# Kernel optimization log

Hardware: AMD Instinct MI355X
Metric: run time of the kernel (lower is better)

The kernel has to match this reference:

```python
import jax, jax.numpy as jnp
import numpy as np

HEADS = 8
DIM_HEAD = 32
EPS = 1e-5


def _rel_index(h, w):
    # matches Attention._generate_relative_index (static, computed on host)
    coords = np.stack(np.meshgrid(np.arange(h), np.arange(w), indexing='ij')).reshape(2, -1)
    rel = coords[:, :, None] - coords[:, None, :]  # [2, n, n]
    rel[0] += h - 1
    rel[1] += w - 1
    rel[0] *= 2 * w - 1
    idx = rel.sum(0).reshape(-1)
    # torch.clamp(relative_index, 0, max_index) -- indices are already in range here
    return jnp.asarray(np.clip(idx, 0, (2 * h - 1) * (2 * w - 1) - 1))


def _layernorm(x, g, b):
    m = jnp.mean(x, axis=-1, keepdims=True)
    v = jnp.var(x, axis=-1, keepdims=True)
    return (x - m) * jax.lax.rsqrt(v + EPS) * g + b


def setup_inputs() -> dict:
    key = jax.random.key(0)
    ks = jax.random.split(key, 6)
    B, C, H, W = 64, 384, 16, 16
    inner = HEADS * DIM_HEAD  # 256
    hid = 4 * C               # 1536
    def nrm(k, shape, s=0.02):
        return jax.random.normal(k, shape, jnp.float32) * s
    return {
        'x': jax.random.normal(ks[0], (B, C, H, W), jnp.float32),
        'ln1_g': jnp.ones((C,), jnp.float32),
        'ln1_b': jnp.zeros((C,), jnp.float32),
        'w_qkv': nrm(ks[1], (C, 3 * inner)),
        'bias_table': nrm(ks[2], ((2 * H - 1) * (2 * W - 1), HEADS)),
        'w_out': nrm(ks[3], (inner, C)),
        'b_out': jnp.zeros((C,), jnp.float32),
        'ln2_g': jnp.ones((C,), jnp.float32),
        'ln2_b': jnp.zeros((C,), jnp.float32),
        'w_ff1': nrm(ks[4], (C, hid)),
        'b_ff1': jnp.zeros((hid,), jnp.float32),
        'w_ff2': nrm(ks[5], (hid, C)),
        'b_ff2': jnp.zeros((C,), jnp.float32),
    }


def reference(x, ln1_g, ln1_b, w_qkv, bias_table, w_out, b_out,
              ln2_g, ln2_b, w_ff1, b_ff1, w_ff2, b_ff2):
    B, C, H, W = x.shape
    n = H * W
    t = x.reshape(B, C, n).transpose(0, 2, 1)  # [B, n, C]

    # --- attention branch (PreNorm(LayerNorm) -> Attention) ---
    a = _layernorm(t, ln1_g, ln1_b)
    qkv = a @ w_qkv  # [B, n, 3*inner]
    q, k, v = jnp.split(qkv, 3, axis=-1)
    def split_heads(z):
        return z.reshape(B, n, HEADS, DIM_HEAD).transpose(0, 2, 1, 3)  # [B, h, n, d]
    q, k, v = split_heads(q), split_heads(k), split_heads(v)
    dots = jnp.einsum('bhid,bhjd->bhij', q, k) * (DIM_HEAD ** -0.5)
    idx = _rel_index(H, W)  # [n*n]
    rel_bias = bias_table[idx].reshape(n, n, HEADS).transpose(2, 0, 1)[None]  # [1, h, n, n]
    attn = jax.nn.softmax(dots + rel_bias, axis=-1)
    o = jnp.einsum('bhij,bhjd->bhid', attn, v)
    o = o.transpose(0, 2, 1, 3).reshape(B, n, HEADS * DIM_HEAD)
    attn_out = o @ w_out + b_out  # to_out Linear (dropout=0)

    # --- feedforward branch (PreNorm(LayerNorm) -> FFN) ---
    f = _layernorm(t, ln2_g, ln2_b)
    f = jax.nn.gelu(f @ w_ff1 + b_ff1, approximate=False) @ w_ff2 + b_ff2

    y = t + attn_out + f  # x_adjusted + attn_out + ff_out
    return y.transpose(0, 2, 1).reshape(B, C, H, W)
```

## Files before the change

kernel.cpp:

```cpp
#include <hip/hip_runtime.h>

typedef __bf16 bf16;
typedef __bf16 bf16x8 __attribute__((ext_vector_type(8)));
typedef float f32x4 __attribute__((ext_vector_type(4)));

__device__ __forceinline__ void gll16(const void* g, void* l) {
    __builtin_amdgcn_global_load_lds((const __attribute__((address_space(1))) void*)g,
                                     (__attribute__((address_space(3))) void*)l, 16, 0, 0);
}

__device__ __forceinline__ float gelu_f(float v) {
    float x2 = v * v;
    float sn = v * fmaf(-0.0713540072f, x2, -1.5957691216f);
    float e  = __expf(sn);
    return v * __builtin_amdgcn_rcpf(1.0f + e);
}

__launch_bounds__(256)
__global__ void prep_kernel(const float* __restrict__ wqkv, const float* __restrict__ wout,
                            const float* __restrict__ wff1, const float* __restrict__ wff2,
                            bf16* __restrict__ wqkvT, bf16* __restrict__ woutT,
                            bf16* __restrict__ wff1T, bf16* __restrict__ wff2T,
                            const float* __restrict__ x,
                            const float* __restrict__ g1, const float* __restrict__ b1,
                            const float* __restrict__ g2, const float* __restrict__ b2,
                            bf16* __restrict__ a, bf16* __restrict__ f) {
    __shared__ __align__(16) float smem[12672 + 512 + 64];
    const int tid = threadIdx.x;
    int g = blockIdx.x;
    if (g < 1536) {
        float (*tl)[33] = (float (*)[33])smem;
        const float* in; bf16* out; int R, Cc, bx, by;
        if (g < 288)       { in = wqkv; out = wqkvT; R = 384;  Cc = 768;  bx = g % 24; by = g / 24; }
        else if (g < 384)  { g -= 288; in = wout; out = woutT; R = 256;  Cc = 384;  bx = g % 12; by = g / 12; }
        else if (g < 960)  { g -= 384; in = wff1; out = wff1T; R = 384;  Cc = 1536; bx = g % 48; by = g / 48; }
        else               { g -= 960; in = wff2; out = wff2T; R = 1536; Cc = 384;  bx = g % 12; by = g / 12; }
        const int c0 = bx * 32, r0 = by * 32;
        const int cl = tid & 31, r8 = tid >> 5;
#pragma unroll
        for (int k = 0; k < 4; k++) {
            int r = k * 8 + r8;
            tl[r][cl] = in[(size_t)(r0 + r) * Cc + c0 + cl];
        }
        __syncthreads();
#pragma unroll
        for (int k = 0; k < 4; k++) {
            int cc = k * 8 + r8;
            out[(size_t)(c0 + cc) * R + r0 + cl] = (bf16)tl[cl][cc];
        }
        return;
    }
    g -= 1536;
    float (*tile)[33] = (float (*)[33])smem;
    float (*S)[32]  = (float (*)[32])(smem + 12672);
    float (*SS)[32] = (float (*)[32])(smem + 12928);
    float* Mn = smem + 13184;
    float* Rs = smem + 13216;
    const int bb = g >> 3;
    const int i0 = (g & 7) * 32;
    {
        const int i_l = tid & 31, c_l = tid >> 5;
        const size_t base = (size_t)bb * 384 * 256 + i0 + i_l;
#pragma unroll 6
        for (int c = c_l; c < 384; c += 8)
            tile[c][i_l] = x[base + (size_t)c * 256];
    }
    __syncthreads();
    {
        const int i_s = tid & 31, p = tid >> 5;
        float s = 0.f, ss = 0.f;
#pragma unroll 6
        for (int j = 0; j < 48; j++) {
            float v = tile[p * 48 + j][i_s];
            s += v; ss += v * v;
        }
        S[p][i_s] = s; SS[p][i_s] = ss;
    }
    __syncthreads();
    if (tid < 32) {
        float t1 = 0.f, t2 = 0.f;
#pragma unroll
        for (int p = 0; p < 8; p++) { t1 += S[p][tid]; t2 += SS[p][tid]; }
        float mean = t1 * (1.0f / 384.0f);
        float var  = t2 * (1.0f / 384.0f) - mean * mean;
        Mn[tid] = mean;
        Rs[tid] = rsqrtf(var + 1e-5f);
    }
    __syncthreads();
    const int lane = tid & 63, w = tid >> 6;
#pragma unroll
    for (int rr = 0; rr < 8; rr++) {
        const int i = w * 8 + rr;
        const float mean = Mn[i], rstd = Rs[i];
        const size_t orow = ((size_t)bb * 256 + i0 + i) * 384;
#pragma unroll
        for (int pass = 0; pass < 6; pass++) {
            const int c = pass * 64 + lane;
            float nh = (tile[c][i] - mean) * rstd;
            a[orow + c] = (bf16)(nh * g1[c] + b1[c]);
            f[orow + c] = (bf16)(nh * g2[c] + b2[c]);
        }
    }
}

template <int EPI>
__launch_bounds__(256)
__global__ void gemm_bt(const bf16* __restrict__ A, const bf16* __restrict__ Bt,
                        const float* __restrict__ bias, bf16* __restrict__ C,
                        int M, int N, int K, int nx) {
    __shared__ bf16 lds[16384];
    bf16* lA = lds;
    bf16* lB = lds + 4096;
    const int tid = threadIdx.x;
    const int g = blockIdx.x;
    const int x = (g >> 3) % nx;
    const int y = (g & 7) + 8 * (g / (8 * nx));
    const int m0 = y * 128, n0 = x * 128;
    const int lane = tid & 63, w = tid >> 6;
    const int l16 = lane & 15, quad = lane >> 4;
    const int wm = (w & 1) * 64, wn = (w >> 1) * 64;

    f32x4 zero = {0.f, 0.f, 0.f, 0.f};
    f32x4 acc[4][4];
#pragma unroll
    for (int i = 0; i < 4; i++)
#pragma unroll
        for (int j = 0; j < 4; j++) acc[i][j] = zero;

    const int c0 = tid, c1 = tid + 256;
    const int r0 = c0 >> 2, k0c = (c0 & 3) * 8;
    const int r1 = c1 >> 2, k1c = (c1 & 3) * 8;
    const bf16* Abase = A + (size_t)m0 * K;
    const bf16* Bbase = Bt + (size_t)n0 * K;

    for (int kb = 0; kb < K; kb += 32) {
        gll16(Abase + (size_t)r0 * K + kb + k0c, lA + c0 * 8);
        gll16(Abase + (size_t)r1 * K + kb + k1c, lA + c1 * 8);
        gll16(Bbase + (size_t)r0 * K + kb + k0c, lB + c0 * 8);
        gll16(Bbase + (size_t)r1 * K + kb + k1c, lB + c1 * 8);
        __syncthreads();
        bf16x8 af[4], bfr[4];
#pragma unroll
        for (int i = 0; i < 4; i++)
            af[i] = *(const bf16x8*)(lA + (wm + i * 16 + l16) * 32 + quad * 8);
#pragma unroll
        for (int j = 0; j < 4; j++)
            bfr[j] = *(const bf16x8*)(lB + (wn + j * 16 + l16) * 32 + quad * 8);
#pragma unroll
        for (int i = 0; i < 4; i++)
#pragma unroll
            for (int j = 0; j < 4; j++)
                acc[i][j] = __builtin_amdgcn_mfma_f32_16x16x32_bf16(af[i], bfr[j], acc[i][j], 0, 0, 0);
        __syncthreads();
    }

#pragma unroll
    for (int j = 0; j < 4; j++) {
        const int col = wn + j * 16 + l16;
        float bv = 0.f;
        if (EPI >= 1) bv = bias[n0 + col];
#pragma unroll
        for (int i = 0; i < 4; i++) {
            const int row0 = wm + i * 16 + quad * 4;
#pragma unroll
            for (int r = 0; r < 4; r++) {
                float v = acc[i][j][r] + bv;
                if (EPI == 2) v = gelu_f(v);
                lds[(row0 + r) * 128 + col] = (bf16)v;
            }
        }
    }
    __syncthreads();
#pragma unroll
    for (int it = 0; it < 8; it++) {
        const int ch = tid + it * 256;
        const int row = ch >> 4, cc = (ch & 15) * 8;
        *(bf16x8*)(C + (size_t)(m0 + row) * N + n0 + cc) = *(const bf16x8*)(lds + row * 128 + cc);
    }
}

#define GEMM64_PROLOGUE_AND_KLOOP                                                   \
    const int tid = threadIdx.x;                                                    \
    const int g = blockIdx.x;                                                       \
    const int x_ = (g >> 3) % nx;                                                   \
    const int y_ = (g & 7) + 8 * (g / (8 * nx));                                    \
    const int m0 = y_ * 128, n0 = x_ * 64;                                          \
    const int lane = tid & 63, w = tid >> 6;                                        \
    const int l16 = lane & 15, quad = lane >> 4;                                    \
    const int wm = (w & 1) * 64, wn = (w >> 1) * 32;                                \
    f32x4 zero = {0.f, 0.f, 0.f, 0.f};                                              \
    f32x4 acc[4][2];                                                                \
    _Pragma("unroll") for (int i = 0; i < 4; i++)                                   \
        _Pragma("unroll") for (int j = 0; j < 2; j++) acc[i][j] = zero;             \
    const int c0 = tid, c1 = tid + 256;                                             \
    const int r0 = c0 >> 2, k0c = (c0 & 3) * 8;                                     \
    const int r1 = c1 >> 2, k1c = (c1 & 3) * 8;                                     \
    const bf16* Abase = A + (size_t)m0 * K;                                         \
    const bf16* Bbase = Bt + (size_t)n0 * K;                                        \
    for (int kb = 0; kb < K; kb += 64) {                                            \
        gll16(Abase + (size_t)r0 * K + kb + k0c,      lA0 + c0 * 8);                \
        gll16(Abase + (size_t)r1 * K + kb + k1c,      lA0 + c1 * 8);                \
        gll16(Abase + (size_t)r0 * K + kb + 32 + k0c, lA1 + c0 * 8);                \
        gll16(Abase + (size_t)r1 * K + kb + 32 + k1c, lA1 + c1 * 8);                \
        gll16(Bbase + (size_t)r0 * K + kb + k0c,      lB0 + c0 * 8);                \
        gll16(Bbase + (size_t)r0 * K + kb + 32 + k0c, lB1 + c0 * 8);                \
        __syncthreads();                                                            \
        bf16x8 af[4], bfr[2];                                                       \
        _Pragma("unroll") for (int i = 0; i < 4; i++)                               \
            af[i] = *(const bf16x8*)(lA0 + (wm + i * 16 + l16) * 32 + quad * 8);    \
        _Pragma("unroll") for (int j = 0; j < 2; j++)                               \
            bfr[j] = *(const bf16x8*)(lB0 + (wn + j * 16 + l16) * 32 + quad * 8);   \
        _Pragma("unroll") for (int i = 0; i < 4; i++)                               \
            _Pragma("unroll") for (int j = 0; j < 2; j++)                           \
                acc[i][j] = __builtin_amdgcn_mfma_f32_16x16x32_bf16(af[i], bfr[j], acc[i][j], 0, 0, 0); \
        _Pragma("unroll") for (int i = 0; i < 4; i++)                               \
            af[i] = *(const bf16x8*)(lA1 + (wm + i * 16 + l16) * 32 + quad * 8);    \
        _Pragma("unroll") for (int j = 0; j < 2; j++)                               \
            bfr[j] = *(const bf16x8*)(lB1 + (wn + j * 16 + l16) * 32 + quad * 8);   \
        _Pragma("unroll") for (int i = 0; i < 4; i++)                               \
            _Pragma("unroll") for (int j = 0; j < 2; j++)                           \
                acc[i][j] = __builtin_amdgcn_mfma_f32_16x16x32_bf16(af[i], bfr[j], acc[i][j], 0, 0, 0); \
        __syncthreads();                                                            \
    }

__launch_bounds__(256)
__global__ void gemm_bt_tr64(const bf16* __restrict__ A, const bf16* __restrict__ Bt,
                             const float* __restrict__ bias, bf16* __restrict__ Ct,
                             int M, int N, int K, int nx) {
    __shared__ bf16 lds[12288];
    bf16* lA0 = lds;
    bf16* lA1 = lds + 4096;
    bf16* lB0 = lds + 8192;
    bf16* lB1 = lds + 10240;
    GEMM64_PROLOGUE_AND_KLOOP
#pragma unroll
    for (int j = 0; j < 2; j++) {
        const int col = wn + j * 16 + l16;
        const float bv = bias[n0 + col];
#pragma unroll
        for (int i = 0; i < 4; i++) {
            const int row0 = wm + i * 16 + quad * 4;
#pragma unroll
            for (int r = 0; r < 4; r++)
                lds[col * 132 + row0 + r] = (bf16)(acc[i][j][r] + bv);
        }
    }
    __syncthreads();
    const int b = m0 >> 8, ib = m0 & 255;
#pragma unroll
    for (int it = 0; it < 4; it++) {
        const int ch = tid + it * 256;
        const int cl = ch >> 4, ic = (ch & 15) * 8;
        *(bf16x8*)(Ct + ((size_t)(b * 384 + n0 + cl) * 256 + ib + ic)) =
            *(const bf16x8*)(lds + cl * 132 + ic);
    }
}

__launch_bounds__(256)
__global__ void gemm_bt_final64(const bf16* __restrict__ A, const bf16* __restrict__ Bt,
                                const float* __restrict__ bias,
                                const float* __restrict__ xres, const bf16* __restrict__ attn_t,
                                float* __restrict__ out, int M, int N, int K, int nx) {
    __shared__ bf16 lds[12288];
    bf16* lA0 = lds;
    bf16* lA1 = lds + 4096;
    bf16* lB0 = lds + 8192;
    bf16* lB1 = lds + 10240;
    GEMM64_PROLOGUE_AND_KLOOP
#pragma unroll
    for (int j = 0; j < 2; j++) {
        const int col = wn + j * 16 + l16;
        const float bv = bias[n0 + col];
#pragma unroll
        for (int i = 0; i < 4; i++) {
            const int row0 = wm + i * 16 + quad * 4;
#pragma unroll
            for (int r = 0; r < 4; r++)
                lds[col * 132 + row0 + r] = (bf16)(acc[i][j][r] + bv);
        }
    }
    __syncthreads();
    const int b = m0 >> 8, ib = m0 & 255;
#pragma unroll
    for (int it = 0; it < 4; it++) {
        const int ch = tid + it * 256;
        const int cl = ch >> 4, ic = (ch & 15) * 8;
        const size_t base = (size_t)(b * 384 + n0 + cl) * 256 + ib + ic;
        bf16x8 ff = *(const bf16x8*)(lds + cl * 132 + ic);
        bf16x8 at = *(const bf16x8*)(attn_t + base);
#pragma unroll
        for (int e = 0; e < 8; e++)
            out[base + e] = xres[base + e] + (float)at[e] + (float)ff[e];
    }
}

__launch_bounds__(256)
__global__ void attn_kernel(const bf16* __restrict__ qkv,
                            const float* __restrict__ btab,
                            bf16* __restrict__ o) {
    __shared__ float sbias[961];
    __shared__ __align__(16) bf16 sK[256 * 32];
    __shared__ __align__(16) bf16 sVt[32][264];
    __shared__ __align__(16) bf16 sP[4][16][264];
    const int tid = threadIdx.x;
    const int g = blockIdx.x;
    const int h  = (g >> 3) & 7;
    const int bb = (g & 7) + 8 * (g >> 6);
    const int lane = tid & 63, w = tid >> 6;
    const int l16 = lane & 15, quad = lane >> 4;
    const size_t qkvb = (size_t)bb * 256 * 768;
    const bf16* Qbase = qkv + qkvb + h * 32;
    const bf16* Kbase = qkv + qkvb + 256 + h * 32;
    const bf16* Vbase = qkv + qkvb + 512 + h * 32;

    for (int e = tid; e < 961; e += 256) sbias[e] = btab[e * 8 + h];
#pragma unroll
    for (int it = 0; it < 4; it++) {
        const int ch = it * 256 + tid;
        const int row = ch >> 2, d8 = (ch & 3) * 8;
        gll16(Kbase + (size_t)row * 768 + d8, sK + ch * 8);
    }
#pragma unroll
    for (int it = 0; it < 4; it++) {
        const int ch = it * 256 + tid;
        const int k = ch >> 2, d8 = (ch & 3) * 8;
        bf16x8 vv = *(const bf16x8*)(Vbase + (size_t)k * 768 + d8);
#pragma unroll
        for (int j = 0; j < 8; j++)
            sVt[d8 + j][k] = vv[j];
    }
    __syncthreads();

    f32x4 zero = {0.f, 0.f, 0.f, 0.f};
    for (int qc = 0; qc < 4; qc++) {
        const int qbase = qc * 64 + w * 16;
        bf16x8 qf = *(const bf16x8*)(Qbase + (size_t)(qbase + l16) * 768 + quad * 8);
        f32x4 s[16];
#pragma unroll
        for (int kt = 0; kt < 16; kt++) {
            bf16x8 kf = *(const bf16x8*)(sK + (kt * 16 + l16) * 32 + quad * 8);
            s[kt] = __builtin_amdgcn_mfma_f32_16x16x32_bf16(qf, kf, zero, 0, 0, 0);
        }
        const int qi0 = qbase + quad * 4;
        float mx[4] = {-1e30f, -1e30f, -1e30f, -1e30f};
#pragma unroll
        for (int kt = 0; kt < 16; kt++) {
            const int j = kt * 16 + l16;
            const int yj = j >> 4, xj = j & 15;
#pragma unroll
            for (int r = 0; r < 4; r++) {
                const int q = qi0 + r;
                const int tix = ((q >> 4) - yj + 15) * 31 + ((q & 15) - xj + 15);
                float v = s[kt][r] * 0.17677669529663687f + sbias[tix];
                s[kt][r] = v;
                mx[r] = fmaxf(mx[r], v);
            }
        }
#pragma unroll
        for (int r = 0; r < 4; r++)
            for (int msk = 1; msk < 16; msk <<= 1)
                mx[r] = fmaxf(mx[r], __shfl_xor(mx[r], msk, 64));
        float sum[4] = {0.f, 0.f, 0.f, 0.f};
#pragma unroll
        for (int kt = 0; kt < 16; kt++)
#pragma unroll
            for (int r = 0; r < 4; r++) {
                float e = __expf(s[kt][r] - mx[r]);
                s[kt][r] = e;
                sum[r] += e;
            }
#pragma unroll
        for (int r = 0; r < 4; r++) {
            for (int msk = 1; msk < 16; msk <<= 1)
                sum[r] += __shfl_xor(sum[r], msk, 64);
            sum[r] = 1.0f / sum[r];
        }
#pragma unroll
        for (int kt = 0; kt < 16; kt++)
#pragma unroll
            for (int r = 0; r < 4; r++)
                sP[w][quad * 4 + r][kt * 16 + l16] = (bf16)(s[kt][r] * sum[r]);
        f32x4 oacc[2];
        oacc[0] = zero; oacc[1] = zero;
#pragma unroll
        for (int ks = 0; ks < 8; ks++) {
            bf16x8 pf = *(const bf16x8*)(&sP[w][l16][ks * 32 + quad * 8]);
#pragma unroll
            for (int dt = 0; dt < 2; dt++) {
                bf16x8 vf = *(const bf16x8*)(&sVt[dt * 16 + l16][ks * 32 + quad * 8]);
                oacc[dt] = __builtin_amdgcn_mfma_f32_16x16x32_bf16(pf, vf, oacc[dt], 0, 0, 0);
            }
        }
#pragma unroll
        for (int dt = 0; dt < 2; dt++)
#pragma unroll
            for (int r = 0; r < 4; r++)
                o[(size_t)(bb * 256 + qbase + quad * 4 + r) * 256 + h * 32 + dt * 16 + l16] = (bf16)oacc[dt][r];
    }
}

extern "C" void kernel_launch(void* const* d_in, const int* in_sizes, int n_in,
                              void* d_out, int out_size, void* d_ws, size_t ws_size,
                              hipStream_t stream) {
    const float* x    = (const float*)d_in[0];
    const float* g1   = (const float*)d_in[1];
    const float* b1   = (const float*)d_in[2];
    const float* wqkv = (const float*)d_in[3];
    const float* btab = (const float*)d_in[4];
    const float* wout = (const float*)d_in[5];
    const float* bout = (const float*)d_in[6];
    const float* g2   = (const float*)d_in[7];
    const float* b2   = (const float*)d_in[8];
    const float* wff1 = (const float*)d_in[9];
    const float* bff1 = (const float*)d_in[10];
    const float* wff2 = (const float*)d_in[11];
    const float* bff2 = (const float*)d_in[12];
    float* out = (float*)d_out;

    bf16* ws = (bf16*)d_ws;
    const size_t NA = 6291456;
    bf16* wqkvT = ws;
    bf16* woutT = wqkvT + 294912;
    bf16* wff1T = woutT + 98304;
    bf16* wff2T = wff1T + 589824;
    bf16* f_buf    = ws + 1572864;
    bf16* attn_t   = f_buf + NA;
    bf16* R        = attn_t + NA;
    bf16* a_buf    = R;
    bf16* qkv_buf  = R + NA;
    bf16* o_buf    = R;
    bf16* ffh_buf  = R;

    dim3 b256(256);
    prep_kernel<<<2048, b256, 0, stream>>>(wqkv, wout, wff1, wff2, wqkvT, woutT, wff1T, wff2T,
                                           x, g1, b1, g2, b2, a_buf, f_buf);

    gemm_bt<0><<<6 * 128, b256, 0, stream>>>(a_buf, wqkvT, nullptr, qkv_buf, 16384, 768, 384, 6);
    attn_kernel<<<512, b256, 0, stream>>>(qkv_buf, btab, o_buf);
    gemm_bt_tr64<<<6 * 128, b256, 0, stream>>>(o_buf, woutT, bout, attn_t, 16384, 384, 256, 6);
    gemm_bt<2><<<12 * 128, b256, 0, stream>>>(f_buf, wff1T, bff1, ffh_buf, 16384, 1536, 384, 12);
    gemm_bt_final64<<<6 * 128, b256, 0, stream>>>(ffh_buf, wff2T, bff2, x, attn_t, out,
                                                  16384, 384, 1536, 6);
}
```

Baseline: 228.8 us.

## Double-buffer LDS staging in GEMM kernels and vectorize final residual store

Converts the GEMM k-loops to double-buffered LDS staging. The next 32-wide K slice is issued via global_load_lds before the MFMA work on the current slice, which removes one barrier per iteration and overlaps load latency with compute. The 64-wide GEMMs drop their 64-deep K step for 32-deep steps with ping-pong buffers. The final epilogue also switches to float4 loads and stores for the residual sum. The risk is that async LDS loads may not be properly awaited before use: the compiler's vmcnt waits and the single barrier must cover the in-flight buffer.

```diff
diff --git a/kernel.cpp b/kernel.cpp
--- a/kernel.cpp
+++ b/kernel.cpp
@@ -109,8 +109,6 @@
                         const float* __restrict__ bias, bf16* __restrict__ C,
                         int M, int N, int K, int nx) {
     __shared__ bf16 lds[16384];
-    bf16* lA = lds;
-    bf16* lB = lds + 4096;
     const int tid = threadIdx.x;
     const int g = blockIdx.x;
     const int x = (g >> 3) % nx;
@@ -133,12 +131,23 @@
     const bf16* Abase = A + (size_t)m0 * K;
     const bf16* Bbase = Bt + (size_t)n0 * K;
 
+#define STAGE128(buf, kb)                                                   \
+    {                                                                       \
+        bf16* lA = lds + (buf) * 8192;                                      \
+        bf16* lB = lA + 4096;                                               \
+        gll16(Abase + (size_t)r0 * K + (kb) + k0c, lA + c0 * 8);            \
+        gll16(Abase + (size_t)r1 * K + (kb) + k1c, lA + c1 * 8);            \
+        gll16(Bbase + (size_t)r0 * K + (kb) + k0c, lB + c0 * 8);            \
+        gll16(Bbase + (size_t)r1 * K + (kb) + k1c, lB + c1 * 8);            \
+    }
+
+    STAGE128(0, 0);
+    __syncthreads();
+    int cur = 0;
     for (int kb = 0; kb < K; kb += 32) {
-        gll16(Abase + (size_t)r0 * K + kb + k0c, lA + c0 * 8);
-        gll16(Abase + (size_t)r1 * K + kb + k1c, lA + c1 * 8);
-        gll16(Bbase + (size_t)r0 * K + kb + k0c, lB + c0 * 8);
-        gll16(Bbase + (size_t)r1 * K + kb + k1c, lB + c1 * 8);
-        __syncthreads();
+        if (kb + 32 < K) STAGE128(cur ^ 1, kb + 32);
+        const bf16* lA = lds + cur * 8192;
+        const bf16* lB = lA + 4096;
         bf16x8 af[4], bfr[4];
 #pragma unroll
         for (int i = 0; i < 4; i++)
@@ -152,7 +161,9 @@
             for (int j = 0; j < 4; j++)
                 acc[i][j] = __builtin_amdgcn_mfma_f32_16x16x32_bf16(af[i], bfr[j], acc[i][j], 0, 0, 0);
         __syncthreads();
-    }
+        cur ^= 1;
+    }
+#undef STAGE128
 
 #pragma unroll
     for (int j = 0; j < 4; j++) {
@@ -195,32 +206,35 @@
     const int c0 = tid, c1 = tid + 256;                                             \
     const int r0 = c0 >> 2, k0c = (c0 & 3) * 8;                                     \
     const int r1 = c1 >> 2, k1c = (c1 & 3) * 8;                                     \
+    const int rB = tid >> 2, kBc = (tid & 3) * 8;                                   \
     const bf16* Abase = A + (size_t)m0 * K;                                         \
     const bf16* Bbase = Bt + (size_t)n0 * K;                                        \
-    for (int kb = 0; kb < K; kb += 64) {                                            \
-        gll16(Abase + (size_t)r0 * K + kb + k0c,      lA0 + c0 * 8);                \
-        gll16(Abase + (size_t)r1 * K + kb + k1c,      lA0 + c1 * 8);                \
-        gll16(Abase + (size_t)r0 * K + kb + 32 + k0c, lA1 + c0 * 8);                \
-        gll16(Abase + (size_t)r1 * K + kb + 32 + k1c, lA1 + c1 * 8);                \
-        gll16(Bbase + (size_t)r0 * K + kb + k0c,      lB0 + c0 * 8);                \
-        gll16(Bbase + (size_t)r0 * K + kb + 32 + k0c, lB1 + c0 * 8);                \
-        __syncthreads();                                                            \
+    STAGE64(0, 0);                                                                  \
+    __syncthreads();                                                                \
+    int cur = 0;                                                                    \
+    for (int kb = 0; kb < K; kb += 32) {                                            \
+        if (kb + 32 < K) STAGE64(cur ^ 1, kb + 32);                                 \
+        const bf16* lA = lds + cur * 6144;                                          \
+        const bf16* lB = lA + 4096;                                                 \
         bf16x8 af[4], bfr[2];                                                       \
         _Pragma("unroll") for (int i = 0; i < 4; i++)                               \
-            af[i] = *(const bf16x8*)(lA0 + (wm + i * 16 + l16) * 32 + quad * 8);    \
+            af[i] = *(const bf16x8*)(lA + (wm + i * 16 + l16) * 32 + quad * 8);     \
         _Pragma("unroll") for (int j = 0; j < 2; j++)                               \
-            bfr[j] = *(const bf16x8*)(lB0 + (wn + j * 16 + l16) * 32 + quad * 8);   \
-        _Pragma("unroll") for (int i = 0; i < 4; i++)                               \
-            _Pragma("unroll") for (int j = 0; j < 2; j++)                           \
-                acc[i][j] = __builtin_amdgcn_mfma_f32_16x16x32_bf16(af[i], bfr[j], acc[i][j], 0, 0, 0); \
-        _Pragma("unroll") for (int i = 0; i < 4; i++)                               \
-            af[i] = *(const bf16x8*)(lA1 + (wm + i * 16 + l16) * 32 + quad * 8);    \
-        _Pragma("unroll") for (int j = 0; j < 2; j++)                               \
-            bfr[j] = *(const bf16x8*)(lB1 + (wn + j * 16 + l16) * 32 + quad * 8);   \
+            bfr[j] = *(const bf16x8*)(lB + (wn + j * 16 + l16) * 32 + quad * 8);    \
         _Pragma("unroll") for (int i = 0; i < 4; i++)                               \
             _Pragma("unroll") for (int j = 0; j < 2; j++)                           \
                 acc[i][j] = __builtin_amdgcn_mfma_f32_16x16x32_bf16(af[i], bfr[j], acc[i][j], 0, 0, 0); \
         __syncthreads();                                                            \
+        cur ^= 1;                                                                   \
+    }
+
+#define STAGE64(buf, kb)                                                            \
+    {                                                                               \
+        bf16* lA = lds + (buf) * 6144;                                              \
+        bf16* lB = lA + 4096;                                                       \
+        gll16(Abase + (size_t)r0 * K + (kb) + k0c, lA + c0 * 8);                    \
+        gll16(Abase + (size_t)r1 * K + (kb) + k1c, lA + c1 * 8);                    \
+        gll16(Bbase + (size_t)rB * K + (kb) + kBc, lB + tid * 8);                   \
     }
 
 __launch_bounds__(256)
@@ -228,10 +242,6 @@
                              const float* __restrict__ bias, bf16* __restrict__ Ct,
                              int M, int N, int K, int nx) {
     __shared__ bf16 lds[12288];
-    bf16* lA0 = lds;
-    bf16* lA1 = lds + 4096;
-    bf16* lB0 = lds + 8192;
-    bf16* lB1 = lds + 10240;
     GEMM64_PROLOGUE_AND_KLOOP
 #pragma unroll
     for (int j = 0; j < 2; j++) {
@@ -262,10 +272,6 @@
                                 const float* __restrict__ xres, const bf16* __restrict__ attn_t,
                                 float* __restrict__ out, int M, int N, int K, int nx) {
     __shared__ bf16 lds[12288];
-    bf16* lA0 = lds;
-    bf16* lA1 = lds + 4096;
-    bf16* lB0 = lds + 8192;
-    bf16* lB1 = lds + 10240;
     GEMM64_PROLOGUE_AND_KLOOP
 #pragma unroll
     for (int j = 0; j < 2; j++) {
@@ -288,9 +294,14 @@
         const size_t base = (size_t)(b * 384 + n0 + cl) * 256 + ib + ic;
         bf16x8 ff = *(const bf16x8*)(lds + cl * 132 + ic);
         bf16x8 at = *(const bf16x8*)(attn_t + base);
-#pragma unroll
-        for (int e = 0; e < 8; e++)
-            out[base + e] = xres[base + e] + (float)at[e] + (float)ff[e];
+        const f32x4* xr = (const f32x4*)(xres + base);
+        f32x4 o0, o1;
+#pragma unroll
+        for (int e = 0; e < 4; e++) o0[e] = xr[0][e] + (float)at[e] + (float)ff[e];
+#pragma unroll
+        for (int e = 0; e < 4; e++) o1[e] = xr[1][e] + (float)at[e + 4] + (float)ff[e + 4];
+        ((f32x4*)(out + base))[0] = o0;
+        ((f32x4*)(out + base))[1] = o1;
     }
 }
 
```

Measured after the change: 229.7 us. About the same (+0.4%).
